# Kernel tuning notes

Hardware: AMD Instinct MI355X
Metric: run time of the kernel (lower is better)

## Reference

```python
import jax, jax.numpy as jnp
import numpy as np

D_MODEL = 256
N = 8192

def setup_inputs() -> dict:
    key = jax.random.key(0)
    k1, k2, k3, k4 = jax.random.split(key, 4)
    x = jax.random.normal(k1, (N, D_MODEL), dtype=jnp.float32)
    # nn.Linear weights: shape [out, in], applied as x @ W.T
    s = 1.0 / np.sqrt(D_MODEL)
    Wq = jax.random.normal(k2, (D_MODEL, D_MODEL), dtype=jnp.float32) * s
    Wk = jax.random.normal(k3, (D_MODEL, D_MODEL), dtype=jnp.float32) * s
    Wv = jax.random.normal(k4, (D_MODEL, D_MODEL), dtype=jnp.float32) * s
    return {"x": x, "Wq": Wq, "Wk": Wk, "Wv": Wv}

def reference(x, Wq, Wk, Wv):
    d_model = Wq.shape[0]
    Q = x @ Wq.T  # [N, d]
    K = x @ Wk.T
    V = x @ Wv.T
    scores = (Q @ K.T) / jnp.sqrt(jnp.asarray(d_model, x.dtype))  # [N, N]
    attn = jax.nn.softmax(scores, axis=-1)  # stable max-sub softmax, same math
    cntx = attn @ V  # [N, d]
    return (cntx, attn)
```

## Files before the change

### kernel.cpp

```cpp
#include <hip/hip_runtime.h>

#define D_MODEL 256
#define NSEQ    8192
#define PV_GROUPS 8

typedef _Float16 half8 __attribute__((ext_vector_type(8)));
typedef _Float16 half4 __attribute__((ext_vector_type(4)));
typedef float    f32x4 __attribute__((ext_vector_type(4)));

__device__ __forceinline__ half8 cvt8(f32x4 a, f32x4 b) {
  half8 h;
  h[0]=(_Float16)a[0]; h[1]=(_Float16)a[1]; h[2]=(_Float16)a[2]; h[3]=(_Float16)a[3];
  h[4]=(_Float16)b[0]; h[5]=(_Float16)b[1]; h[6]=(_Float16)b[2]; h[7]=(_Float16)b[3];
  return h;
}

__device__ __forceinline__ half8 load8_f32(const float* p) {
  f32x4 a = *(const f32x4*)p;
  f32x4 b = *(const f32x4*)(p + 4);
  return cvt8(a, b);
}


__global__ __launch_bounds__(64, 3) void qkv_kernel(
    const float* __restrict__ x, const float* __restrict__ Wq,
    const float* __restrict__ Wk, const float* __restrict__ Wv,
    _Float16* __restrict__ QK16, _Float16* __restrict__ VT)
{
  const int lane = threadIdx.x & 63;
  const int c    = lane & 15;
  const int quad = lane >> 4;
  const int M0   = blockIdx.x * 64;
  const int Nblk = blockIdx.y * 64;
  const int widx = Nblk >> 8;
  const int nloc = Nblk & 255;
  const float* W = (widx == 0) ? Wq : (widx == 1 ? Wk : Wv);

  f32x4 acc[4][4] = {};
  for (int k0 = 0; k0 < D_MODEL; k0 += 32) {
    half8 af[4], bf[4];
#pragma unroll
    for (int mt = 0; mt < 4; ++mt)
      af[mt] = load8_f32(&x[(size_t)(M0 + mt*16 + c) * D_MODEL + k0 + quad*8]);
#pragma unroll
    for (int nt = 0; nt < 4; ++nt)
      bf[nt] = load8_f32(&W[(size_t)(nloc + nt*16 + c) * D_MODEL + k0 + quad*8]);
#pragma unroll
    for (int mt = 0; mt < 4; ++mt)
#pragma unroll
      for (int nt = 0; nt < 4; ++nt)
        acc[mt][nt] = __builtin_amdgcn_mfma_f32_16x16x32_f16(af[mt], bf[nt], acc[mt][nt], 0, 0, 0);
  }

  if (widx < 2) {
#pragma unroll
    for (int mt = 0; mt < 4; ++mt)
#pragma unroll
      for (int nt = 0; nt < 4; ++nt) {
        const int col  = widx * 256 + nloc + nt*16 + c;
        const int row0 = M0 + mt*16 + quad*4;
#pragma unroll
        for (int r = 0; r < 4; ++r)
          QK16[(size_t)(row0 + r) * 512 + col] = (_Float16)acc[mt][nt][r];
      }
  } else {
#pragma unroll
    for (int mt = 0; mt < 4; ++mt)
#pragma unroll
      for (int nt = 0; nt < 4; ++nt) {
        const int d  = nloc + nt*16 + c;
        const int m0 = M0 + mt*16 + quad*4;
        half4 h;
        h[0]=(_Float16)acc[mt][nt][0]; h[1]=(_Float16)acc[mt][nt][1];
        h[2]=(_Float16)acc[mt][nt][2]; h[3]=(_Float16)acc[mt][nt][3];
        *(half4*)&VT[(size_t)d * NSEQ + m0] = h;
      }
  }
}

template<bool P16>
__global__ __launch_bounds__(256, 3) void score_kernel(
    const _Float16* __restrict__ QK16, void* __restrict__ Pout,
    float* __restrict__ lsum)
{
  const int tid  = threadIdx.x;
  const int lane = tid & 63;
  const int wave = tid >> 6;
  const int c    = lane & 15;
  const int quad = lane >> 4;
  const int M0   = blockIdx.x * 128 + (wave >> 1) * 64;
  const int N0   = blockIdx.y * 128 + (wave & 1) * 64;

  f32x4 acc[4][4] = {};
  half8 afA[4], bfA[4], afB[4], bfB[4];

  auto ld = [&](half8 (&af)[4], half8 (&bf)[4], int k0) {
#pragma unroll
    for (int mt = 0; mt < 4; ++mt)
      af[mt] = *(const half8*)&QK16[(size_t)(M0 + mt*16 + c) * 512 + k0 + quad*8];
#pragma unroll
    for (int nt = 0; nt < 4; ++nt)
      bf[nt] = *(const half8*)&QK16[(size_t)(N0 + nt*16 + c) * 512 + 256 + k0 + quad*8];
  };
  auto mm = [&](half8 (&af)[4], half8 (&bf)[4]) {
#pragma unroll
    for (int mt = 0; mt < 4; ++mt)
#pragma unroll
      for (int nt = 0; nt < 4; ++nt)
        acc[mt][nt] = __builtin_amdgcn_mfma_f32_16x16x32_f16(af[mt], bf[nt], acc[mt][nt], 0, 0, 0);
  };

  ld(afA, bfA, 0);
#pragma unroll
  for (int k0 = 0; k0 < 256; k0 += 64) {
    ld(afB, bfB, k0 + 32);
    mm(afA, bfA);
    if (k0 + 64 < 256) ld(afA, bfA, k0 + 64);
    mm(afB, bfB);
  }

  float psum[4][4] = {};
#pragma unroll
  for (int mt = 0; mt < 4; ++mt) {
    const size_t tq = (size_t)((M0 + mt*16) >> 4);
#pragma unroll
    for (int nt = 0; nt < 4; ++nt) {
      const size_t tj   = (size_t)((N0 >> 5) + (nt >> 1));
      const size_t base = (tq * 256 + tj) * 512
                        + (size_t)(((nt*2 + (c>>3)) & 3) * 128 + quad*32 + (c & 7));
#pragma unroll
      for (int r = 0; r < 4; ++r) {
        const float p = __expf(acc[mt][nt][r] * 0.0625f);
        psum[mt][r] += p;
        if constexpr (P16) {
          ((_Float16*)Pout)[base + r*8] = (_Float16)p;
        } else {
          const size_t idx = (size_t)(M0 + mt*16 + quad*4 + r) * NSEQ + N0 + nt*16 + c;
          ((float*)Pout)[idx] = p;
        }
      }
    }
  }

#pragma unroll
  for (int mt = 0; mt < 4; ++mt)
#pragma unroll
    for (int r = 0; r < 4; ++r) {
      float v = psum[mt][r];
      v += __shfl_xor(v, 1);
      v += __shfl_xor(v, 2);
      v += __shfl_xor(v, 4);
      v += __shfl_xor(v, 8);
      if (c == 0) atomicAdd(&lsum[M0 + mt*16 + quad*4 + r], v);
    }
}

__global__ __launch_bounds__(256) void pv_kernel_p16(
    const _Float16* __restrict__ P16F, float* __restrict__ attn,
    const float* __restrict__ lsum, const _Float16* __restrict__ VT,
    float* __restrict__ cntx)
{
  const int tid  = threadIdx.x;
  const int lane = tid & 63;
  const int wave = tid >> 6;
  const int c    = lane & 15;
  const int quad = lane >> 4;
  const int M0   = blockIdx.x * 32;
  const int jb   = blockIdx.y * (NSEQ / PV_GROUPS);
  const int je   = jb + NSEQ / PV_GROUPS;
  const int D0   = wave * 64;
  const int nq   = tid >> 3;
  const int ng   = tid & 7;

  const float nscale = 1.0f / lsum[M0 + nq];

  const size_t tqA = (size_t)(M0 >> 4);
  const size_t tqN = (size_t)((M0 + nq) >> 4);
  const int    ofsN = ((ng & 3) * 16 + ((M0 + nq) & 15)) * 8;

  f32x4 acc[2][4] = {};
  for (int j0 = jb; j0 < je; j0 += 64) {
    const size_t tj0 = (size_t)(j0 >> 5);

    half8 af[2][2];
#pragma unroll
    for (int mt = 0; mt < 2; ++mt)
#pragma unroll
      for (int ks = 0; ks < 2; ++ks)
        af[mt][ks] = *(const half8*)&P16F[((tqA + mt) * 256 + tj0 + ks) * 512 + lane * 8];

    half8 bf[4][2];
#pragma unroll
    for (int ks = 0; ks < 2; ++ks)
#pragma unroll
      for (int nt = 0; nt < 4; ++nt)
        bf[nt][ks] = *(const half8*)&VT[(size_t)(D0 + nt*16 + c) * NSEQ + j0 + ks*32 + quad*8];

    {
      const half8 v = *(const half8*)&P16F[(tqN * 256 + tj0 + (ng >> 2)) * 512 + ofsN];
      f32x4 w0, w1;
#pragma unroll
      for (int r = 0; r < 4; ++r) {
        w0[r] = (float)v[r]     * nscale;
        w1[r] = (float)v[r + 4] * nscale;
      }
      float* ar = attn + (size_t)(M0 + nq) * NSEQ + j0 + ng*8;
      *(f32x4*)ar       = w0;
      *(f32x4*)(ar + 4) = w1;
    }

#pragma unroll
    for (int ks = 0; ks < 2; ++ks)
#pragma unroll
      for (int mt = 0; mt < 2; ++mt)
#pragma unroll
        for (int nt = 0; nt < 4; ++nt)
          acc[mt][nt] = __builtin_amdgcn_mfma_f32_16x16x32_f16(af[mt][ks], bf[nt][ks], acc[mt][nt], 0, 0, 0);
  }

#pragma unroll
  for (int mt = 0; mt < 2; ++mt)
#pragma unroll
    for (int r = 0; r < 4; ++r) {
      const float s = 1.0f / lsum[M0 + mt*16 + quad*4 + r];
#pragma unroll
      for (int nt = 0; nt < 4; ++nt)
        atomicAdd(&cntx[(size_t)(M0 + mt*16 + quad*4 + r) * D_MODEL + D0 + nt*16 + c],
                  acc[mt][nt][r] * s);
    }
}

__global__ __launch_bounds__(256) void pv_kernel_f32(
    const float* __restrict__ Pin, float* __restrict__ attn,
    const float* __restrict__ lsum, const _Float16* __restrict__ VT,
    float* __restrict__ cntx)
{
  __shared__ float linv[32];
  const int tid  = threadIdx.x;
  const int lane = tid & 63;
  const int wave = tid >> 6;
  const int c    = lane & 15;
  const int quad = lane >> 4;
  const int M0   = blockIdx.x * 32;
  const int jb   = blockIdx.y * (NSEQ / PV_GROUPS);
  const int je   = jb + NSEQ / PV_GROUPS;
  const int D0   = wave * 64;
  const int nr   = tid >> 3;
  const int ncol = (tid & 7) * 8;

  if (tid < 32) linv[tid] = 1.0f / lsum[M0 + tid];
  __syncthreads();
  const float nscale = linv[nr];

  f32x4 acc[2][4] = {};
  for (int j0 = jb; j0 < je; j0 += 64) {
    const float* pr = Pin + (size_t)(M0 + nr) * NSEQ + j0 + ncol;
    f32x4 np0 = *(const f32x4*)pr;
    f32x4 np1 = *(const f32x4*)(pr + 4);

    half8 af[2][2], bf[4][2];
#pragma unroll
    for (int h = 0; h < 2; ++h) {
#pragma unroll
      for (int mt = 0; mt < 2; ++mt) {
        const float* pa = Pin + (size_t)(M0 + mt*16 + c) * NSEQ + j0 + h*32 + quad*8;
        af[mt][h] = cvt8(*(const f32x4*)pa, *(const f32x4*)(pa + 4));
      }
#pragma unroll
      for (int nt = 0; nt < 4; ++nt)
        bf[nt][h] = *(const half8*)&VT[(size_t)(D0 + nt*16 + c) * NSEQ + j0 + h*32 + quad*8];
    }

    __syncthreads();

    float* ar = attn + (size_t)(M0 + nr) * NSEQ + j0 + ncol;
    *(f32x4*)ar       = np0 * nscale;
    *(f32x4*)(ar + 4) = np1 * nscale;

#pragma unroll
    for (int h = 0; h < 2; ++h)
#pragma unroll
      for (int mt = 0; mt < 2; ++mt)
#pragma unroll
        for (int nt = 0; nt < 4; ++nt)
          acc[mt][nt] = __builtin_amdgcn_mfma_f32_16x16x32_f16(af[mt][h], bf[nt][h], acc[mt][nt], 0, 0, 0);
  }

#pragma unroll
  for (int mt = 0; mt < 2; ++mt)
#pragma unroll
    for (int r = 0; r < 4; ++r) {
      const float s = linv[mt*16 + quad*4 + r];
#pragma unroll
      for (int nt = 0; nt < 4; ++nt)
        atomicAdd(&cntx[(size_t)(M0 + mt*16 + quad*4 + r) * D_MODEL + D0 + nt*16 + c],
                  acc[mt][nt][r] * s);
    }
}

extern "C" void kernel_launch(void* const* d_in, const int* in_sizes, int n_in,
                              void* d_out, int out_size, void* d_ws, size_t ws_size,
                              hipStream_t stream)
{
  const float* x  = (const float*)d_in[0];
  const float* Wq = (const float*)d_in[1];
  const float* Wk = (const float*)d_in[2];
  const float* Wv = (const float*)d_in[3];

  float* cntx = (float*)d_out;
  float* attn = cntx + (size_t)NSEQ * D_MODEL;

  _Float16* QK16 = (_Float16*)d_ws;
  _Float16* VT   = QK16 + (size_t)NSEQ * 512;
  float*    lsum = (float*)(VT + (size_t)D_MODEL * NSEQ);
  _Float16* P16F = (_Float16*)(lsum + NSEQ);

  const size_t base_bytes = (size_t)NSEQ*512*2 + (size_t)D_MODEL*NSEQ*2 + (size_t)NSEQ*4;
  const bool big_ws = ws_size >= base_bytes + (size_t)NSEQ * NSEQ * 2;

  hipMemsetAsync(cntx, 0, sizeof(float) * (size_t)NSEQ * D_MODEL, stream);
  hipMemsetAsync(lsum, 0, sizeof(float) * NSEQ, stream);

  qkv_kernel<<<dim3(128, 12), 64, 0, stream>>>(x, Wq, Wk, Wv, QK16, VT);

  if (big_ws) {
    score_kernel<true><<<dim3(64, 64), 256, 0, stream>>>(QK16, (void*)P16F, lsum);
    pv_kernel_p16<<<dim3(NSEQ/32, PV_GROUPS), 256, 0, stream>>>(P16F, attn, lsum, VT, cntx);
  } else {
    score_kernel<false><<<dim3(64, 64), 256, 0, stream>>>(QK16, (void*)attn, lsum);
    pv_kernel_f32<<<dim3(NSEQ/32, PV_GROUPS), 256, 0, stream>>>(attn, attn, lsum, VT, cntx);
  }
}
```

Baseline: 635.4 us.

## Stage score tiles through LDS and split PV into GEMM, normalize, and reduce kernels

The score kernel now loads Q and K tiles into LDS with global_load_lds double buffering and shares them across the four waves, instead of each wave loading from global memory directly. The PV stage is split into three kernels when workspace allows: a larger-tile GEMM that writes per-group partial context buffers (no atomics), a separate kernel that normalizes P into attn, and a reduction kernel that sums the partials and applies 1/lsum. The QKV projection uses smaller 32x32 tiles with more blocks for better occupancy. The split adds extra launches and partial-buffer traffic in exchange for removing cntx atomics and the memset.

```diff
diff --git a/kernel.cpp b/kernel.cpp
--- a/kernel.cpp
+++ b/kernel.cpp
@@ -7,6 +7,9 @@
 typedef _Float16 half8 __attribute__((ext_vector_type(8)));
 typedef _Float16 half4 __attribute__((ext_vector_type(4)));
 typedef float    f32x4 __attribute__((ext_vector_type(4)));
+
+typedef __attribute__((address_space(1))) const void* gptr_t;
+typedef __attribute__((address_space(3))) void*       lptr_t;
 
 __device__ __forceinline__ half8 cvt8(f32x4 a, f32x4 b) {
   half8 h;
@@ -22,7 +25,7 @@
 }
 
 
-__global__ __launch_bounds__(64, 3) void qkv_kernel(
+__global__ __launch_bounds__(64, 6) void qkv_kernel(
     const float* __restrict__ x, const float* __restrict__ Wq,
     const float* __restrict__ Wk, const float* __restrict__ Wv,
     _Float16* __restrict__ QK16, _Float16* __restrict__ VT)
@@ -30,33 +33,32 @@
   const int lane = threadIdx.x & 63;
   const int c    = lane & 15;
   const int quad = lane >> 4;
-  const int M0   = blockIdx.x * 64;
-  const int Nblk = blockIdx.y * 64;
-  const int widx = Nblk >> 8;
-  const int nloc = Nblk & 255;
+  const int M0   = blockIdx.x * 32;
+  const int widx = blockIdx.y >> 3;
+  const int nloc = (blockIdx.y & 7) * 32;
   const float* W = (widx == 0) ? Wq : (widx == 1 ? Wk : Wv);
 
-  f32x4 acc[4][4] = {};
+  f32x4 acc[2][2] = {};
   for (int k0 = 0; k0 < D_MODEL; k0 += 32) {
-    half8 af[4], bf[4];
-#pragma unroll
-    for (int mt = 0; mt < 4; ++mt)
+    half8 af[2], bf[2];
+#pragma unroll
+    for (int mt = 0; mt < 2; ++mt)
       af[mt] = load8_f32(&x[(size_t)(M0 + mt*16 + c) * D_MODEL + k0 + quad*8]);
 #pragma unroll
-    for (int nt = 0; nt < 4; ++nt)
+    for (int nt = 0; nt < 2; ++nt)
       bf[nt] = load8_f32(&W[(size_t)(nloc + nt*16 + c) * D_MODEL + k0 + quad*8]);
 #pragma unroll
-    for (int mt = 0; mt < 4; ++mt)
-#pragma unroll
-      for (int nt = 0; nt < 4; ++nt)
+    for (int mt = 0; mt < 2; ++mt)
+#pragma unroll
+      for (int nt = 0; nt < 2; ++nt)
         acc[mt][nt] = __builtin_amdgcn_mfma_f32_16x16x32_f16(af[mt], bf[nt], acc[mt][nt], 0, 0, 0);
   }
 
   if (widx < 2) {
 #pragma unroll
-    for (int mt = 0; mt < 4; ++mt)
-#pragma unroll
-      for (int nt = 0; nt < 4; ++nt) {
+    for (int mt = 0; mt < 2; ++mt)
+#pragma unroll
+      for (int nt = 0; nt < 2; ++nt) {
         const int col  = widx * 256 + nloc + nt*16 + c;
         const int row0 = M0 + mt*16 + quad*4;
 #pragma unroll
@@ -65,9 +67,9 @@
       }
   } else {
 #pragma unroll
-    for (int mt = 0; mt < 4; ++mt)
-#pragma unroll
-      for (int nt = 0; nt < 4; ++nt) {
+    for (int mt = 0; mt < 2; ++mt)
+#pragma unroll
+      for (int nt = 0; nt < 2; ++nt) {
         const int d  = nloc + nt*16 + c;
         const int m0 = M0 + mt*16 + quad*4;
         half4 h;
@@ -79,53 +81,63 @@
 }
 
 template<bool P16>
-__global__ __launch_bounds__(256, 3) void score_kernel(
+__global__ __launch_bounds__(256) void score_kernel(
     const _Float16* __restrict__ QK16, void* __restrict__ Pout,
     float* __restrict__ lsum)
 {
+  __shared__ alignas(16) _Float16 Qs[2][8][512];
+  __shared__ alignas(16) _Float16 Ks[2][8][512];
   const int tid  = threadIdx.x;
   const int lane = tid & 63;
   const int wave = tid >> 6;
   const int c    = lane & 15;
   const int quad = lane >> 4;
-  const int M0   = blockIdx.x * 128 + (wave >> 1) * 64;
-  const int N0   = blockIdx.y * 128 + (wave & 1) * 64;
+  const int wr   = wave >> 1;
+  const int wc   = wave & 1;
+  const int M0   = blockIdx.x * 128;
+  const int N0   = blockIdx.y * 128;
+  const int mb   = M0 + wr * 64;
+  const int nb   = N0 + wc * 64;
+
+  auto stage = [&](int buf, int k0) {
+#pragma unroll
+    for (int s = 0; s < 2; ++s) {
+      const int t = wave * 2 + s;
+      const _Float16* qsrc = &QK16[(size_t)(M0 + t*16 + (lane & 15)) * 512 + k0 + (lane >> 4) * 8];
+      __builtin_amdgcn_global_load_lds((gptr_t)qsrc, (lptr_t)&Qs[buf][t][0], 16, 0, 0);
+      const _Float16* ksrc = &QK16[(size_t)(N0 + t*16 + (lane & 15)) * 512 + 256 + k0 + (lane >> 4) * 8];
+      __builtin_amdgcn_global_load_lds((gptr_t)ksrc, (lptr_t)&Ks[buf][t][0], 16, 0, 0);
+    }
+  };
 
   f32x4 acc[4][4] = {};
-  half8 afA[4], bfA[4], afB[4], bfB[4];
-
-  auto ld = [&](half8 (&af)[4], half8 (&bf)[4], int k0) {
+  stage(0, 0);
+  __syncthreads();
+  for (int it = 0; it < 8; ++it) {
+    const int buf = it & 1;
+    if (it < 7) stage(buf ^ 1, (it + 1) * 32);
+    half8 af[4], bf[4];
 #pragma unroll
     for (int mt = 0; mt < 4; ++mt)
-      af[mt] = *(const half8*)&QK16[(size_t)(M0 + mt*16 + c) * 512 + k0 + quad*8];
+      af[mt] = *(const half8*)&Qs[buf][wr*4 + mt][lane * 8];
 #pragma unroll
     for (int nt = 0; nt < 4; ++nt)
-      bf[nt] = *(const half8*)&QK16[(size_t)(N0 + nt*16 + c) * 512 + 256 + k0 + quad*8];
-  };
-  auto mm = [&](half8 (&af)[4], half8 (&bf)[4]) {
+      bf[nt] = *(const half8*)&Ks[buf][wc*4 + nt][lane * 8];
 #pragma unroll
     for (int mt = 0; mt < 4; ++mt)
 #pragma unroll
       for (int nt = 0; nt < 4; ++nt)
         acc[mt][nt] = __builtin_amdgcn_mfma_f32_16x16x32_f16(af[mt], bf[nt], acc[mt][nt], 0, 0, 0);
-  };
-
-  ld(afA, bfA, 0);
-#pragma unroll
-  for (int k0 = 0; k0 < 256; k0 += 64) {
-    ld(afB, bfB, k0 + 32);
-    mm(afA, bfA);
-    if (k0 + 64 < 256) ld(afA, bfA, k0 + 64);
-    mm(afB, bfB);
+    __syncthreads();
   }
 
   float psum[4][4] = {};
 #pragma unroll
   for (int mt = 0; mt < 4; ++mt) {
-    const size_t tq = (size_t)((M0 + mt*16) >> 4);
+    const size_t tq = (size_t)((mb >> 4) + mt);
 #pragma unroll
     for (int nt = 0; nt < 4; ++nt) {
-      const size_t tj   = (size_t)((N0 >> 5) + (nt >> 1));
+      const size_t tj   = (size_t)((nb >> 5) + (nt >> 1));
       const size_t base = (tq * 256 + tj) * 512
                         + (size_t)(((nt*2 + (c>>3)) & 3) * 128 + quad*32 + (c & 7));
 #pragma unroll
@@ -135,7 +147,7 @@
         if constexpr (P16) {
           ((_Float16*)Pout)[base + r*8] = (_Float16)p;
         } else {
-          const size_t idx = (size_t)(M0 + mt*16 + quad*4 + r) * NSEQ + N0 + nt*16 + c;
+          const size_t idx = (size_t)(mb + mt*16 + quad*4 + r) * NSEQ + nb + nt*16 + c;
           ((float*)Pout)[idx] = p;
         }
       }
@@ -151,8 +163,119 @@
       v += __shfl_xor(v, 2);
       v += __shfl_xor(v, 4);
       v += __shfl_xor(v, 8);
-      if (c == 0) atomicAdd(&lsum[M0 + mt*16 + quad*4 + r], v);
-    }
+      if (c == 0) atomicAdd(&lsum[mb + mt*16 + quad*4 + r], v);
+    }
+}
+
+__global__ __launch_bounds__(256) void pv_gemm_kernel(
+    const _Float16* __restrict__ P16F, const _Float16* __restrict__ VT,
+    float* __restrict__ cpart, int jlen)
+{
+  __shared__ alignas(16) _Float16 As[2][8][512];
+  const int tid  = threadIdx.x;
+  const int lane = tid & 63;
+  const int wave = tid >> 6;
+  const int c    = lane & 15;
+  const int quad = lane >> 4;
+  const int M0   = blockIdx.x * 64;
+  const int gy   = blockIdx.y;
+  const int jb   = gy * jlen;
+  const int D0   = wave * 64;
+  const size_t tqA = (size_t)(M0 >> 4);
+
+  auto stage = [&](int buf, int j0) {
+    const size_t tj0 = (size_t)(j0 >> 5);
+#pragma unroll
+    for (int s = 0; s < 2; ++s) {
+      const int t = wave * 2 + s;
+      const _Float16* src = &P16F[((tqA + (t >> 1)) * 256 + tj0 + (t & 1)) * 512 + lane * 8];
+      __builtin_amdgcn_global_load_lds((gptr_t)src, (lptr_t)&As[buf][t][0], 16, 0, 0);
+    }
+  };
+
+  f32x4 acc[4][4] = {};
+  stage(0, jb);
+  __syncthreads();
+  const int iters = jlen >> 6;
+  for (int it = 0; it < iters; ++it) {
+    const int buf = it & 1;
+    const int j0  = jb + it * 64;
+    if (it + 1 < iters) stage(buf ^ 1, j0 + 64);
+
+    half8 af[4][2];
+#pragma unroll
+    for (int mt = 0; mt < 4; ++mt)
+#pragma unroll
+      for (int ks = 0; ks < 2; ++ks)
+        af[mt][ks] = *(const half8*)&As[buf][mt*2 + ks][lane * 8];
+
+    half8 bf[4][2];
+#pragma unroll
+    for (int ks = 0; ks < 2; ++ks)
+#pragma unroll
+      for (int nt = 0; nt < 4; ++nt)
+        bf[nt][ks] = *(const half8*)&VT[(size_t)(D0 + nt*16 + c) * NSEQ + j0 + ks*32 + quad*8];
+
+#pragma unroll
+    for (int ks = 0; ks < 2; ++ks)
+#pragma unroll
+      for (int mt = 0; mt < 4; ++mt)
+#pragma unroll
+        for (int nt = 0; nt < 4; ++nt)
+          acc[mt][nt] = __builtin_amdgcn_mfma_f32_16x16x32_f16(af[mt][ks], bf[nt][ks], acc[mt][nt], 0, 0, 0);
+    __syncthreads();
+  }
+
+  float* out = cpart + (size_t)gy * NSEQ * D_MODEL;
+#pragma unroll
+  for (int mt = 0; mt < 4; ++mt)
+#pragma unroll
+    for (int nt = 0; nt < 4; ++nt)
+#pragma unroll
+      for (int r = 0; r < 4; ++r)
+        out[(size_t)(M0 + mt*16 + quad*4 + r) * D_MODEL + D0 + nt*16 + c] = acc[mt][nt][r];
+}
+
+__global__ __launch_bounds__(256, 8) void norm_kernel(
+    const _Float16* __restrict__ P16F, const float* __restrict__ lsum,
+    float* __restrict__ attn)
+{
+  const int tid = threadIdx.x;
+  const int q   = tid >> 4;
+  const int gl  = tid & 15;
+  const int bx  = blockIdx.x;
+  const int j0  = blockIdx.y * 1024;
+
+  const float nscale = 1.0f / lsum[bx*16 + q];
+  const size_t tbase = (size_t)bx * 256 + (size_t)(j0 >> 5);
+
+#pragma unroll
+  for (int it = 0; it < 8; ++it) {
+    const int g = gl + it * 16;
+    const half8 v = *(const half8*)&P16F[(tbase + (g >> 2)) * 512 + ((g & 3) * 16 + q) * 8];
+    f32x4 w0, w1;
+#pragma unroll
+    for (int r = 0; r < 4; ++r) {
+      w0[r] = (float)v[r]     * nscale;
+      w1[r] = (float)v[r + 4] * nscale;
+    }
+    float* ar = attn + (size_t)(bx*16 + q) * NSEQ + j0 + g*8;
+    *(f32x4*)ar       = w0;
+    *(f32x4*)(ar + 4) = w1;
+  }
+}
+
+__global__ __launch_bounds__(256, 8) void reduce_kernel(
+    const float* __restrict__ cpart, const float* __restrict__ lsum,
+    float* __restrict__ cntx, int g)
+{
+  const int idx4 = blockIdx.x * 256 + threadIdx.x;
+  const int row  = idx4 >> 6;
+  const float s  = 1.0f / lsum[row];
+  f32x4 v = {};
+  for (int gi = 0; gi < g; ++gi)
+    v += *(const f32x4*)&cpart[(size_t)gi * NSEQ * D_MODEL + (size_t)idx4 * 4];
+  *(f32x4*)&cntx[(size_t)idx4 * 4] = v * s;
 }
 
 __global__ __launch_bounds__(256) void pv_kernel_p16(
@@ -173,7 +296,6 @@
   const int ng   = tid & 7;
 
   const float nscale = 1.0f / lsum[M0 + nq];
-
   const size_t tqA = (size_t)(M0 >> 4);
   const size_t tqN = (size_t)((M0 + nq) >> 4);
   const int    ofsN = ((ng & 3) * 16 + ((M0 + nq) & 15)) * 8;
@@ -181,21 +303,18 @@
   f32x4 acc[2][4] = {};
   for (int j0 = jb; j0 < je; j0 += 64) {
     const size_t tj0 = (size_t)(j0 >> 5);
-
     half8 af[2][2];
 #pragma unroll
     for (int mt = 0; mt < 2; ++mt)
 #pragma unroll
       for (int ks = 0; ks < 2; ++ks)
         af[mt][ks] = *(const half8*)&P16F[((tqA + mt) * 256 + tj0 + ks) * 512 + lane * 8];
-
     half8 bf[4][2];
 #pragma unroll
     for (int ks = 0; ks < 2; ++ks)
 #pragma unroll
       for (int nt = 0; nt < 4; ++nt)
         bf[nt][ks] = *(const half8*)&VT[(size_t)(D0 + nt*16 + c) * NSEQ + j0 + ks*32 + quad*8];
-
     {
       const half8 v = *(const half8*)&P16F[(tqN * 256 + tj0 + (ng >> 2)) * 512 + ofsN];
       f32x4 w0, w1;
@@ -208,7 +327,6 @@
       *(f32x4*)ar       = w0;
       *(f32x4*)(ar + 4) = w1;
     }
-
 #pragma unroll
     for (int ks = 0; ks < 2; ++ks)
 #pragma unroll
@@ -314,19 +432,32 @@
   _Float16* VT   = QK16 + (size_t)NSEQ * 512;
   float*    lsum = (float*)(VT + (size_t)D_MODEL * NSEQ);
   _Float16* P16F = (_Float16*)(lsum + NSEQ);
+  float*    cpart = (float*)(P16F + (size_t)NSEQ * NSEQ);
 
   const size_t base_bytes = (size_t)NSEQ*512*2 + (size_t)D_MODEL*NSEQ*2 + (size_t)NSEQ*4;
-  const bool big_ws = ws_size >= base_bytes + (size_t)NSEQ * NSEQ * 2;
-
-  hipMemsetAsync(cntx, 0, sizeof(float) * (size_t)NSEQ * D_MODEL, stream);
+  const size_t p16_bytes  = (size_t)NSEQ * NSEQ * 2;
+  const size_t part_bytes = (size_t)NSEQ * D_MODEL * 4;
+
+  int g = 0;
+  for (int gt = 8; gt >= 2; gt >>= 1)
+    if (ws_size >= base_bytes + p16_bytes + (size_t)gt * part_bytes) { g = gt; break; }
+  const bool big_ws = ws_size >= base_bytes + p16_bytes;
+
   hipMemsetAsync(lsum, 0, sizeof(float) * NSEQ, stream);
 
-  qkv_kernel<<<dim3(128, 12), 64, 0, stream>>>(x, Wq, Wk, Wv, QK16, VT);
-
-  if (big_ws) {
+  qkv_kernel<<<dim3(256, 24), 64, 0, stream>>>(x, Wq, Wk, Wv, QK16, VT);
+
+  if (g >= 2) {
+    score_kernel<true><<<dim3(64, 64), 256, 0, stream>>>(QK16, (void*)P16F, lsum);
+    pv_gemm_kernel<<<dim3(128, g), 256, 0, stream>>>(P16F, VT, cpart, NSEQ / g);
+    norm_kernel<<<dim3(512, 8), 256, 0, stream>>>(P16F, lsum, attn);
+    reduce_kernel<<<dim3(NSEQ * D_MODEL / 1024), 256, 0, stream>>>(cpart, lsum, cntx, g);
+  } else if (big_ws) {
+    hipMemsetAsync(cntx, 0, sizeof(float) * (size_t)NSEQ * D_MODEL, stream);
     score_kernel<true><<<dim3(64, 64), 256, 0, stream>>>(QK16, (void*)P16F, lsum);
     pv_kernel_p16<<<dim3(NSEQ/32, PV_GROUPS), 256, 0, stream>>>(P16F, attn, lsum, VT, cntx);
   } else {
+    hipMemsetAsync(cntx, 0, sizeof(float) * (size_t)NSEQ * D_MODEL, stream);
     score_kernel<false><<<dim3(64, 64), 256, 0, stream>>>(QK16, (void*)attn, lsum);
     pv_kernel_f32<<<dim3(NSEQ/32, PV_GROUPS), 256, 0, stream>>>(attn, attn, lsum, VT, cntx);
   }
```

Result: faster. 557.8 us (-12.2%).
